# Kernel tuning notes

Hardware: AMD Instinct MI355X
Metric: run time of the kernel (lower is better)

Reference implementation:

```python
import jax, jax.numpy as jnp
import numpy as np
import math

N_HEADS = 16


def _rope(t, cos, sin):
    # t: [B, S, H, d_k] with d_k paired as (even, odd) -> complex multiply by cos+i*sin
    B, S, H, dk = t.shape
    t = t.reshape(B, S, H, dk // 2, 2)
    t0, t1 = t[..., 0], t[..., 1]
    c = cos[None, :S, None, :]
    s = sin[None, :S, None, :]
    out = jnp.stack([t0 * c - t1 * s, t0 * s + t1 * c], axis=-1)
    return out.reshape(B, S, H, dk)


def setup_inputs() -> dict:
    key = jax.random.key(0)
    ks = jax.random.split(key, 6)
    B, S, D = 2, 2048, 2048
    dk = D // N_HEADS  # 128
    x = jax.random.normal(ks[0], (B, S, D), dtype=jnp.float32)
    # standard RoPE angle table
    inv_freq = 1.0 / (10000.0 ** (np.arange(0, dk, 2, dtype=np.float32) / dk))  # [dk/2]
    t = np.arange(S, dtype=np.float32)
    ang = np.outer(t, inv_freq)  # [S, dk/2]
    freqs_cos = jnp.asarray(np.cos(ang), dtype=jnp.float32)
    freqs_sin = jnp.asarray(np.sin(ang), dtype=jnp.float32)
    # additive causal mask [1,1,S,S]
    causal = jnp.tril(jnp.ones((S, S), dtype=bool))
    mask = jnp.where(causal, 0.0, -1e9).astype(jnp.float32)[None, None]
    wscale = 1.0 / math.sqrt(D)
    Wq = jax.random.normal(ks[1], (D, D), dtype=jnp.float32) * wscale
    Wk = jax.random.normal(ks[2], (D, D), dtype=jnp.float32) * wscale
    Wv = jax.random.normal(ks[3], (D, D), dtype=jnp.float32) * wscale
    Wo = jax.random.normal(ks[4], (D, D), dtype=jnp.float32) * wscale
    return {"x": x, "freqs_cos": freqs_cos, "freqs_sin": freqs_sin, "mask": mask,
            "Wq": Wq, "Wk": Wk, "Wv": Wv, "Wo": Wo}


def reference(x, freqs_cos, freqs_sin, mask, Wq, Wk, Wv, Wo):
    B, S, D = x.shape
    H = N_HEADS
    dk = D // H
    scale = math.sqrt(dk)
    # nn.Linear(w) applies x @ w.T
    Q = (x @ Wq.T).reshape(B, S, H, dk)
    K = (x @ Wk.T).reshape(B, S, H, dk)
    V = (x @ Wv.T).reshape(B, S, H, dk)
    Q = _rope(Q, freqs_cos, freqs_sin)
    K = _rope(K, freqs_cos, freqs_sin)
    new_kv_cache = (K, V)  # kv_cache=None path: cache is just current K, V
    # [B, H, S, dk]
    Qh = Q.transpose(0, 2, 1, 3)
    Kh = K.transpose(0, 2, 1, 3)
    Vh = V.transpose(0, 2, 1, 3)
    scores = jnp.einsum('bhqd,bhkd->bhqk', Qh, Kh) / scale + mask
    attn = jax.nn.softmax(scores, axis=-1)  # dropout=0 (eval)
    ctx = jnp.einsum('bhqk,bhkd->bhqd', attn, Vh)
    ctx = ctx.transpose(0, 2, 1, 3).reshape(B, S, D)
    output = ctx @ Wo.T
    return output, new_kv_cache[0], new_kv_cache[1]
```

## Files before the change

### kernel.cpp

```cpp
#include <hip/hip_runtime.h>
#include <hip/hip_bf16.h>

#define SEQ   2048
#define DIM   2048
#define NH    16
#define DKH   128
#define BATCH 2
#define MROWS (BATCH * SEQ)
#define NQT   (SEQ / 64)

using bf16 = __hip_bfloat16;
typedef __attribute__((ext_vector_type(8))) short short8;
typedef __attribute__((ext_vector_type(4))) short short4v;
typedef __attribute__((ext_vector_type(4))) float floatx4;

union BfBits { bf16 h; short s; };

__device__ __forceinline__ void gl_lds16(const bf16* g, bf16* l) {
  __builtin_amdgcn_global_load_lds(
      (__attribute__((address_space(1))) void*)(g),
      (__attribute__((address_space(3))) void*)(l), 16, 0, 0);
}

#define S_BAR  __builtin_amdgcn_s_barrier()
#define VMCNT6 do { asm volatile("s_waitcnt vmcnt(6)" ::: "memory"); __builtin_amdgcn_sched_barrier(0); } while (0)
#define VMCNT0 do { asm volatile("s_waitcnt vmcnt(0)" ::: "memory"); __builtin_amdgcn_sched_barrier(0); } while (0)
#define LGKM0  do { asm volatile("s_waitcnt lgkmcnt(0)" ::: "memory"); __builtin_amdgcn_sched_barrier(0); } while (0)

__global__ __launch_bounds__(256) void cast5_kernel(const float* __restrict__ x,
                                                    const float* __restrict__ wq,
                                                    const float* __restrict__ wk,
                                                    const float* __restrict__ wv,
                                                    const float* __restrict__ wo,
                                                    bf16* __restrict__ dst,
                                                    int nX4, int nW4, int nTot) {
  int i = blockIdx.x * 256 + threadIdx.x;
  if (i >= nTot) return;
  const float* src;
  int off;
  int j = i - nX4;
  if (j < 0) { src = x; off = i; }
  else {
    int wsel = j >> 20;
    off = j & (nW4 - 1);
    src = (wsel == 0) ? wq : (wsel == 1) ? wk : (wsel == 2) ? wv : wo;
  }
  float4 v = reinterpret_cast<const float4*>(src)[off];
  __hip_bfloat162 h01, h23;
  h01.x = __float2bfloat16(v.x); h01.y = __float2bfloat16(v.y);
  h23.x = __float2bfloat16(v.z); h23.y = __float2bfloat16(v.w);
  reinterpret_cast<__hip_bfloat162*>(dst)[i * 2 + 0] = h01;
  reinterpret_cast<__hip_bfloat162*>(dst)[i * 2 + 1] = h23;
}

#define BUFE (256 * 64 + 128 * 64)

template <int ROWS>
__device__ __forceinline__ void stage_swz(const bf16* __restrict__ G, bf16* lds,
                                          int row0, int k0, int w, int l) {
  const int rr = w * 8 + (l >> 3);
  const int cc = ((l & 7) * 8) ^ ((l >> 3) * 8);
#pragma unroll
  for (int u = 0; u < ROWS / 64; ++u)
    gl_lds16(G + (size_t)(row0 + u * 64 + rr) * DIM + k0 + cc,
             lds + (u * 64 + w * 8) * 64);
}

template <int MODE>
__global__ __launch_bounds__(512, 2) void gemm256(const bf16* __restrict__ A,
                                                  const bf16* __restrict__ Bw,
                                                  bf16* __restrict__ Qraw,
                                                  float* __restrict__ Kout,
                                                  float* __restrict__ Vout) {
  __shared__ bf16 smem[3 * BUFE];

  const int t = threadIdx.x;
  const int w = t >> 6, l = t & 63;
  const int lr = l & 15, quad = l >> 4;
  const int wr = w >> 2;
  const int wc = w & 3;
  const int m0 = blockIdx.y * 256;
  const int n0g = blockIdx.x * 128;

  const int cb = ((quad * 8) ^ ((lr & 7) * 8));

  floatx4 acc[8][2];
#pragma unroll
  for (int mi = 0; mi < 8; ++mi)
#pragma unroll
    for (int nj = 0; nj < 2; ++nj) acc[mi][nj] = (floatx4){0.f, 0.f, 0.f, 0.f};

  const int NT = DIM / 64;

  stage_swz<256>(A, smem, m0, 0, w, l);
  stage_swz<128>(Bw, smem + 256 * 64, n0g, 0, w, l);
  stage_swz<256>(A, smem + BUFE, m0, 64, w, l);
  stage_swz<128>(Bw, smem + BUFE + 256 * 64, n0g, 64, w, l);
  VMCNT6;
  S_BAR;

  for (int kt = 0; kt < NT; ++kt) {
    const bf16* la = smem + (kt % 3) * BUFE;
    const bf16* lb = la + 256 * 64;
    bf16* stg = smem + ((kt + 2) % 3) * BUFE;
    const bool do_stage = (kt + 2 < NT);

    short8 bfr[2][2];
#pragma unroll
    for (int nj = 0; nj < 2; ++nj) {
      int rb = (wc * 32 + nj * 16 + lr) * 64;
      bfr[nj][0] = *reinterpret_cast<const short8*>(lb + rb + cb);
      bfr[nj][1] = *reinterpret_cast<const short8*>(lb + rb + (cb ^ 32));
    }
    short8 af[4][2];
#pragma unroll
    for (int i = 0; i < 4; ++i) {
      int ra = (wr * 128 + i * 16 + lr) * 64;
      af[i][0] = *reinterpret_cast<const short8*>(la + ra + cb);
      af[i][1] = *reinterpret_cast<const short8*>(la + ra + (cb ^ 32));
    }
    if (do_stage) stage_swz<256>(A, stg, m0, (kt + 2) * 64, w, l);
    LGKM0;
    __builtin_amdgcn_s_setprio(1);
#pragma unroll
    for (int i = 0; i < 4; ++i)
#pragma unroll
      for (int nj = 0; nj < 2; ++nj) {
        acc[i][nj] = __builtin_amdgcn_mfma_f32_16x16x32_bf16(
            af[i][0], bfr[nj][0], acc[i][nj], 0, 0, 0);
        acc[i][nj] = __builtin_amdgcn_mfma_f32_16x16x32_bf16(
            af[i][1], bfr[nj][1], acc[i][nj], 0, 0, 0);
      }
    __builtin_amdgcn_s_setprio(0);

#pragma unroll
    for (int i = 0; i < 4; ++i) {
      int ra = (wr * 128 + (i + 4) * 16 + lr) * 64;
      af[i][0] = *reinterpret_cast<const short8*>(la + ra + cb);
      af[i][1] = *reinterpret_cast<const short8*>(la + ra + (cb ^ 32));
    }
    if (do_stage) stage_swz<128>(Bw, stg + 256 * 64, n0g, (kt + 2) * 64, w, l);
    LGKM0;
    __builtin_amdgcn_s_setprio(1);
#pragma unroll
    for (int i = 0; i < 4; ++i)
#pragma unroll
      for (int nj = 0; nj < 2; ++nj) {
        acc[i + 4][nj] = __builtin_amdgcn_mfma_f32_16x16x32_bf16(
            af[i][0], bfr[nj][0], acc[i + 4][nj], 0, 0, 0);
        acc[i + 4][nj] = __builtin_amdgcn_mfma_f32_16x16x32_bf16(
            af[i][1], bfr[nj][1], acc[i + 4][nj], 0, 0, 0);
      }
    __builtin_amdgcn_s_setprio(0);

    if (do_stage) { VMCNT6; } else { VMCNT0; }
    S_BAR;
  }

#pragma unroll
  for (int mi = 0; mi < 8; ++mi)
#pragma unroll
    for (int nj = 0; nj < 2; ++nj) {
      int rg = m0 + wr * 128 + mi * 16 + quad * 4;
      if constexpr (MODE == 0) {
        const int region = n0g >> 11;
        int lcol = (n0g & 2047) + wc * 32 + nj * 16 + lr;
#pragma unroll
        for (int rr2 = 0; rr2 < 4; ++rr2) {
          size_t idx = (size_t)(rg + rr2) * DIM + lcol;
          if (region == 0)      Qraw[idx] = __float2bfloat16(acc[mi][nj][rr2]);
          else if (region == 1) Kout[idx] = acc[mi][nj][rr2];
          else                  Vout[idx] = acc[mi][nj][rr2];
        }
      } else {
        int lcol = n0g + wc * 32 + nj * 16 + lr;
#pragma unroll
        for (int rr2 = 0; rr2 < 4; ++rr2)
          Kout[(size_t)(rg + rr2) * DIM + lcol] = acc[mi][nj][rr2];
      }
    }
}

__global__ __launch_bounds__(256) void rope_q(const bf16* __restrict__ Qraw,
                                              const float* __restrict__ cosT,
                                              const float* __restrict__ sinT,
                                              bf16* __restrict__ Qb) {
  int g = blockIdx.x * 256 + threadIdx.x;
  int p = g & 63;
  int r = g >> 6;
  int h = r & 15;
  int s = (r >> 4) & (SEQ - 1);
  int b = r >> 15;
  __hip_bfloat162 v = reinterpret_cast<const __hip_bfloat162*>(Qraw)[g];
  float x0 = __bfloat162float(v.x), x1 = __bfloat162float(v.y);
  float c = cosT[s * 64 + p], sn = sinT[s * 64 + p];
  __hip_bfloat162 o;
  o.x = __float2bfloat16(x0 * c - x1 * sn);
  o.y = __float2bfloat16(x0 * sn + x1 * c);
  reinterpret_cast<__hip_bfloat162*>(Qb)[((size_t)(b * NH + h) * SEQ + s) * 64 + p] = o;
}

__global__ __launch_bounds__(256) void rope_k(float* __restrict__ Kf,
                                              const float* __restrict__ cosT,
                                              const float* __restrict__ sinT,
                                              bf16* __restrict__ Kb) {
  int g = blockIdx.x * 256 + threadIdx.x;
  int p = g & 63;
  int r = g >> 6;
  int h = r & 15;
  int s = (r >> 4) & (SEQ - 1);
  int b = r >> 15;
  float2 v = reinterpret_cast<const float2*>(Kf)[g];
  float c = cosT[s * 64 + p], sn = sinT[s * 64 + p];
  float o0 = v.x * c - v.y * sn;
  float o1 = v.x * sn + v.y * c;
  reinterpret_cast<float2*>(Kf)[g] = make_float2(o0, o1);
  __hip_bfloat162 ob;
  ob.x = __float2bfloat16(o0);
  ob.y = __float2bfloat16(o1);
  reinterpret_cast<__hip_bfloat162*>(Kb)[((size_t)(b * NH + h) * SEQ + s) * 64 + p] = ob;
}

__global__ __launch_bounds__(256) void vt_kernel(const float* __restrict__ V,
                                                 bf16* __restrict__ Vt) {
  __shared__ float tile[32][33];
  const int s0 = blockIdx.x * 32;
  const int d0 = blockIdx.y * 32;
  const int bh = blockIdx.z;
  const int b = bh >> 4, h = bh & 15;
  const int t = threadIdx.x;
  const int row = t >> 3, c4 = (t & 7) * 4;

  float4 v = *reinterpret_cast<const float4*>(
      V + (size_t)(b * SEQ + s0 + row) * DIM + h * DKH + d0 + c4);
  tile[row][c4 + 0] = v.x; tile[row][c4 + 1] = v.y;
  tile[row][c4 + 2] = v.z; tile[row][c4 + 3] = v.w;
  __syncthreads();

  short4v ov;
#pragma unroll
  for (int i = 0; i < 4; ++i) {
    BfBits u; u.h = __float2bfloat16(tile[c4 + i][row]);
    ov[i] = u.s;
  }
  *reinterpret_cast<short4v*>(Vt + ((size_t)(b * NH + h) * DKH + d0 + row) * SEQ + s0 + c4) = ov;
}

__global__ __launch_bounds__(256) void attn_mfma(const bf16* __restrict__ Qb,
                                                 const bf16* __restrict__ Kb,
                                                 const bf16* __restrict__ Vt,
                                                 bf16* __restrict__ ctx) {
  const int bx = blockIdx.x;
  const int h = blockIdx.y;
  const int b = blockIdx.z;
  const int t = threadIdx.x;
  const int w = t >> 6, lane = t & 63;
  const int lr = lane & 15, quad = lane >> 4;

  __shared__ short Ks[64 * 136];
  __shared__ short Vs[128 * 72];
  __shared__ short Ps[4 * 16 * 72];

  const float scale2 = 0.08838834764831845f * 1.44269504f;
  const float THR = 11.5413f;
  const size_t headQK = (size_t)(b * NH + h) * SEQ * DKH;

  for (int pass = 0; pass < 2; ++pass) {
    const int qt = pass ? bx : (NQT - 1 - bx);

    short8 qa[4];
    {
      const short* qbase = (const short*)Qb + headQK + (size_t)(qt * 64 + w * 16 + lr) * DKH;
#pragma unroll
      for (int kk = 0; kk < 4; ++kk)
        qa[kk] = *reinterpret_cast<const short8*>(qbase + kk * 32 + quad * 8);
    }

    floatx4 o[8];
#pragma unroll
    for (int n = 0; n < 8; ++n) o[n] = (floatx4){0.f, 0.f, 0.f, 0.f};
    float m[4] = {-1e30f, -1e30f, -1e30f, -1e30f};
    float l[4] = {0.f, 0.f, 0.f, 0.f};

    for (int kt = 0; kt <= qt; ++kt) {
      {
        const short* kbase = (const short*)Kb + headQK + (size_t)(kt * 64) * DKH;
#pragma unroll
        for (int u = 0; u < 4; ++u) {
          int c = t + 256 * u;
          *reinterpret_cast<int4*>(Ks + (c >> 4) * 136 + (c & 15) * 8) =
              *reinterpret_cast<const int4*>(kbase + c * 8);
        }
        const short* vbase = (const short*)Vt + (size_t)(b * NH + h) * DKH * SEQ + kt * 64;
#pragma unroll
        for (int u = 0; u < 4; ++u) {
          int c = t + 256 * u;
          *reinterpret_cast<int4*>(Vs + (c >> 3) * 72 + (c & 7) * 8) =
              *reinterpret_cast<const int4*>(vbase + (size_t)(c >> 3) * SEQ + (c & 7) * 8);
        }
      }
      __syncthreads();

      floatx4 sj[4];
#pragma unroll
      for (int j = 0; j < 4; ++j) sj[j] = (floatx4){0.f, 0.f, 0.f, 0.f};
#pragma unroll
      for (int j = 0; j < 4; ++j)
#pragma unroll
        for (int kk = 0; kk < 4; ++kk) {
          short8 kb = *reinterpret_cast<const short8*>(Ks + (j * 16 + lr) * 136 + kk * 32 + quad * 8);
          sj[j] = __builtin_amdgcn_mfma_f32_16x16x32_bf16(qa[kk], kb, sj[j], 0, 0, 0);
        }

      float sc[4][4];
#pragma unroll
      for (int j = 0; j < 4; ++j)
#pragma unroll
        for (int r = 0; r < 4; ++r) sc[j][r] = sj[j][r] * scale2;
      if (kt == qt) {
#pragma unroll
        for (int j = 0; j < 4; ++j) {
          int col = kt * 64 + j * 16 + lr;
#pragma unroll
          for (int r = 0; r < 4; ++r) {
            int rowg = qt * 64 + w * 16 + quad * 4 + r;
            if (col > rowg) sc[j][r] = -1e9f;
          }
        }
      }

#pragma unroll
      for (int r = 0; r < 4; ++r) {
        float mx = fmaxf(fmaxf(sc[0][r], sc[1][r]), fmaxf(sc[2][r], sc[3][r]));
        mx = fmaxf(mx, __shfl_xor(mx, 1, 16));
        mx = fmaxf(mx, __shfl_xor(mx, 2, 16));
        mx = fmaxf(mx, __shfl_xor(mx, 4, 16));
        mx = fmaxf(mx, __shfl_xor(mx, 8, 16));
        if (!__all(mx - m[r] <= THR)) {
          float mnew = fmaxf(m[r], mx);
          float alpha = __builtin_amdgcn_exp2f(m[r] - mnew);
          l[r] *= alpha;
#pragma unroll
          for (int n = 0; n < 8; ++n) o[n][r] *= alpha;
          m[r] = mnew;
        }
        float rs = 0.f;
#pragma unroll
        for (int j = 0; j < 4; ++j) {
          float p = __builtin_amdgcn_exp2f(sc[j][r] - m[r]);
          rs += p;
          BfBits u; u.h = __float2bfloat16(p);
          Ps[(w * 16 + quad * 4 + r) * 72 + j * 16 + lr] = u.s;
        }
        rs += __shfl_xor(rs, 1, 16);
        rs += __shfl_xor(rs, 2, 16);
        rs += __shfl_xor(rs, 4, 16);
        rs += __shfl_xor(rs, 8, 16);
        l[r] += rs;
      }

      short8 pa0 = *reinterpret_cast<const short8*>(Ps + (w * 16 + lr) * 72 + quad * 8);
      short8 pa1 = *reinterpret_cast<const short8*>(Ps + (w * 16 + lr) * 72 + 32 + quad * 8);
#pragma unroll
      for (int n = 0; n < 8; ++n) {
        short8 vb0 = *reinterpret_cast<const short8*>(Vs + (n * 16 + lr) * 72 + quad * 8);
        short8 vb1 = *reinterpret_cast<const short8*>(Vs + (n * 16 + lr) * 72 + 32 + quad * 8);
        o[n] = __builtin_amdgcn_mfma_f32_16x16x32_bf16(pa0, vb0, o[n], 0, 0, 0);
        o[n] = __builtin_amdgcn_mfma_f32_16x16x32_bf16(pa1, vb1, o[n], 0, 0, 0);
      }
      __syncthreads();
    }

    float inv[4];
#pragma unroll
    for (int r = 0; r < 4; ++r) inv[r] = 1.0f / l[r];
#pragma unroll
    for (int r = 0; r < 4; ++r) {
      size_t mrow = (size_t)b * SEQ + qt * 64 + w * 16 + quad * 4 + r;
      bf16* dst = ctx + mrow * DIM + h * DKH;
#pragma unroll
      for (int n = 0; n < 8; ++n)
        dst[n * 16 + lr] = __float2bfloat16(o[n][r] * inv[r]);
    }
  }
}

extern "C" void kernel_launch(void* const* d_in, const int* in_sizes, int n_in,
                              void* d_out, int out_size, void* d_ws, size_t ws_size,
                              hipStream_t stream) {
  const float* x = (const float*)d_in[0];
  const float* fcos = (const float*)d_in[1];
  const float* fsin = (const float*)d_in[2];
  const float* Wq = (const float*)d_in[4];
  const float* Wk = (const float*)d_in[5];
  const float* Wv = (const float*)d_in[6];
  const float* Wo = (const float*)d_in[7];

  float* out = (float*)d_out;
  float* Kout = out + (size_t)MROWS * DIM;
  float* Vout = Kout + (size_t)MROWS * DIM;

  const size_t MD = (size_t)MROWS * DIM;
  const size_t DD = (size_t)DIM * DIM;
  bf16* xb   = (bf16*)d_ws;
  bf16* Wqb  = xb + MD;
  bf16* Wkb  = Wqb + DD;
  bf16* Wvb  = Wkb + DD;
  bf16* Wob  = Wvb + DD;
  bf16* Qraw = Wob + DD;
  bf16* Qb   = Qraw + MD;
  bf16* Kb   = Qb + MD;
  bf16* Vt   = Kb + MD;
  bf16* ctxb = Qraw;

  const int nXD4 = MROWS * DIM / 4;
  const int nWD4 = DIM * DIM / 4;
  const int nTot = nXD4 + 4 * nWD4;
  cast5_kernel<<<nTot / 256, 256, 0, stream>>>(x, Wq, Wk, Wv, Wo, xb, nXD4, nWD4, nTot);

  dim3 gq(3 * DIM / 128, MROWS / 256);
  gemm256<0><<<gq, 512, 0, stream>>>(xb, Wqb, Qraw, Kout, Vout);

  const int npairs = MROWS * DIM / 2;
  rope_q<<<npairs / 256, 256, 0, stream>>>(Qraw, fcos, fsin, Qb);
  rope_k<<<npairs / 256, 256, 0, stream>>>(Kout, fcos, fsin, Kb);

  dim3 gv(SEQ / 32, DKH / 32, BATCH * NH);
  vt_kernel<<<gv, 256, 0, stream>>>(Vout, Vt);

  dim3 ga(NQT / 2, NH, BATCH);
  attn_mfma<<<ga, 256, 0, stream>>>(Qb, Kb, Vt, ctxb);

  dim3 go(DIM / 128, MROWS / 256);
  gemm256<1><<<go, 512, 0, stream>>>(ctxb, Wob, (bf16*)nullptr, out, (float*)nullptr);
}
```

Baseline: 468.7 us.

## Double-buffer K/V tiles in attention with XOR swizzle and merge post-processing kernels

The attention kernel now prefetches the next K/V tile into registers and stores it into a second LDS buffer while the current tile is consumed, so global load latency overlaps MFMA work. Padded LDS rows are replaced with an XOR swizzle to avoid bank conflicts without padding. The RoPE-Q, RoPE-K and V-transpose kernels are merged into one launch with block-index dispatch to cut launch overhead. The cost is more registers and doubled K/V LDS use, which may lower occupancy.

```diff
diff --git a/kernel.cpp b/kernel.cpp
--- a/kernel.cpp
+++ b/kernel.cpp
@@ -181,69 +181,76 @@
     }
 }
 
-__global__ __launch_bounds__(256) void rope_q(const bf16* __restrict__ Qraw,
-                                              const float* __restrict__ cosT,
-                                              const float* __restrict__ sinT,
-                                              bf16* __restrict__ Qb) {
-  int g = blockIdx.x * 256 + threadIdx.x;
-  int p = g & 63;
-  int r = g >> 6;
-  int h = r & 15;
-  int s = (r >> 4) & (SEQ - 1);
-  int b = r >> 15;
-  __hip_bfloat162 v = reinterpret_cast<const __hip_bfloat162*>(Qraw)[g];
-  float x0 = __bfloat162float(v.x), x1 = __bfloat162float(v.y);
-  float c = cosT[s * 64 + p], sn = sinT[s * 64 + p];
-  __hip_bfloat162 o;
-  o.x = __float2bfloat16(x0 * c - x1 * sn);
-  o.y = __float2bfloat16(x0 * sn + x1 * c);
-  reinterpret_cast<__hip_bfloat162*>(Qb)[((size_t)(b * NH + h) * SEQ + s) * 64 + p] = o;
-}
-
-__global__ __launch_bounds__(256) void rope_k(float* __restrict__ Kf,
-                                              const float* __restrict__ cosT,
-                                              const float* __restrict__ sinT,
-                                              bf16* __restrict__ Kb) {
-  int g = blockIdx.x * 256 + threadIdx.x;
-  int p = g & 63;
-  int r = g >> 6;
-  int h = r & 15;
-  int s = (r >> 4) & (SEQ - 1);
-  int b = r >> 15;
-  float2 v = reinterpret_cast<const float2*>(Kf)[g];
-  float c = cosT[s * 64 + p], sn = sinT[s * 64 + p];
-  float o0 = v.x * c - v.y * sn;
-  float o1 = v.x * sn + v.y * c;
-  reinterpret_cast<float2*>(Kf)[g] = make_float2(o0, o1);
-  __hip_bfloat162 ob;
-  ob.x = __float2bfloat16(o0);
-  ob.y = __float2bfloat16(o1);
-  reinterpret_cast<__hip_bfloat162*>(Kb)[((size_t)(b * NH + h) * SEQ + s) * 64 + p] = ob;
-}
-
-__global__ __launch_bounds__(256) void vt_kernel(const float* __restrict__ V,
-                                                 bf16* __restrict__ Vt) {
-  __shared__ float tile[32][33];
-  const int s0 = blockIdx.x * 32;
-  const int d0 = blockIdx.y * 32;
-  const int bh = blockIdx.z;
-  const int b = bh >> 4, h = bh & 15;
-  const int t = threadIdx.x;
-  const int row = t >> 3, c4 = (t & 7) * 4;
-
-  float4 v = *reinterpret_cast<const float4*>(
-      V + (size_t)(b * SEQ + s0 + row) * DIM + h * DKH + d0 + c4);
-  tile[row][c4 + 0] = v.x; tile[row][c4 + 1] = v.y;
-  tile[row][c4 + 2] = v.z; tile[row][c4 + 3] = v.w;
-  __syncthreads();
-
-  short4v ov;
-#pragma unroll
-  for (int i = 0; i < 4; ++i) {
-    BfBits u; u.h = __float2bfloat16(tile[c4 + i][row]);
-    ov[i] = u.s;
-  }
-  *reinterpret_cast<short4v*>(Vt + ((size_t)(b * NH + h) * DKH + d0 + row) * SEQ + s0 + c4) = ov;
+#define NRB ((MROWS * DIM / 2) / 256)
+
+__global__ __launch_bounds__(256) void postproc(const bf16* __restrict__ Qraw,
+                                                float* __restrict__ Kf,
+                                                const float* __restrict__ cosT,
+                                                const float* __restrict__ sinT,
+                                                bf16* __restrict__ Qb,
+                                                bf16* __restrict__ Kb,
+                                                const float* __restrict__ V,
+                                                bf16* __restrict__ Vt) {
+  int bid = blockIdx.x;
+  if (bid < NRB) {
+    int g = bid * 256 + threadIdx.x;
+    int p = g & 63;
+    int r = g >> 6;
+    int h = r & 15;
+    int s = (r >> 4) & (SEQ - 1);
+    int b = r >> 15;
+    __hip_bfloat162 v = reinterpret_cast<const __hip_bfloat162*>(Qraw)[g];
+    float x0 = __bfloat162float(v.x), x1 = __bfloat162float(v.y);
+    float c = cosT[s * 64 + p], sn = sinT[s * 64 + p];
+    __hip_bfloat162 o;
+    o.x = __float2bfloat16(x0 * c - x1 * sn);
+    o.y = __float2bfloat16(x0 * sn + x1 * c);
+    reinterpret_cast<__hip_bfloat162*>(Qb)[((size_t)(b * NH + h) * SEQ + s) * 64 + p] = o;
+    return;
+  }
+  bid -= NRB;
+  if (bid < NRB) {
+    int g = bid * 256 + threadIdx.x;
+    int p = g & 63;
+    int r = g >> 6;
+    int h = r & 15;
+    int s = (r >> 4) & (SEQ - 1);
+    int b = r >> 15;
+    float2 v = reinterpret_cast<const float2*>(Kf)[g];
+    float c = cosT[s * 64 + p], sn = sinT[s * 64 + p];
+    float o0 = v.x * c - v.y * sn;
+    float o1 = v.x * sn + v.y * c;
+    reinterpret_cast<float2*>(Kf)[g] = make_float2(o0, o1);
+    __hip_bfloat162 ob;
+    ob.x = __float2bfloat16(o0);
+    ob.y = __float2bfloat16(o1);
+    reinterpret_cast<__hip_bfloat162*>(Kb)[((size_t)(b * NH + h) * SEQ + s) * 64 + p] = ob;
+    return;
+  }
+  bid -= NRB;
+  {
+    __shared__ float tile[32][33];
+    const int s0 = (bid & 63) * 32;
+    const int d0 = ((bid >> 6) & 3) * 32;
+    const int bh = bid >> 8;
+    const int b = bh >> 4, h = bh & 15;
+    const int t = threadIdx.x;
+    const int row = t >> 3, c4 = (t & 7) * 4;
+
+    float4 v = *reinterpret_cast<const float4*>(
+        V + (size_t)(b * SEQ + s0 + row) * DIM + h * DKH + d0 + c4);
+    tile[row][c4 + 0] = v.x; tile[row][c4 + 1] = v.y;
+    tile[row][c4 + 2] = v.z; tile[row][c4 + 3] = v.w;
+    __syncthreads();
+
+    short4v ov;
+#pragma unroll
+    for (int i = 0; i < 4; ++i) {
+      BfBits u; u.h = __float2bfloat16(tile[c4 + i][row]);
+      ov[i] = u.s;
+    }
+    *reinterpret_cast<short4v*>(Vt + ((size_t)(b * NH + h) * DKH + d0 + row) * SEQ + s0 + c4) = ov;
+  }
 }
 
 __global__ __launch_bounds__(256) void attn_mfma(const bf16* __restrict__ Qb,
@@ -256,14 +263,38 @@
   const int t = threadIdx.x;
   const int w = t >> 6, lane = t & 63;
   const int lr = lane & 15, quad = lane >> 4;
-
-  __shared__ short Ks[64 * 136];
-  __shared__ short Vs[128 * 72];
+  const int kswz = 8 * (lr & 7);
+
+  __shared__ short Ks[2][64 * 128];
+  __shared__ short Vs[2][128 * 64];
   __shared__ short Ps[4 * 16 * 72];
 
   const float scale2 = 0.08838834764831845f * 1.44269504f;
   const float THR = 11.5413f;
   const size_t headQK = (size_t)(b * NH + h) * SEQ * DKH;
+  const short* kbase0 = (const short*)Kb + headQK;
+  const short* vbase0 = (const short*)Vt + (size_t)(b * NH + h) * DKH * SEQ;
+
+  int4 kreg[4], vreg[4];
+
+  auto LD = [&](int kt) {
+#pragma unroll
+    for (int u = 0; u < 4; ++u) {
+      int c = t + 256 * u;
+      kreg[u] = *reinterpret_cast<const int4*>(kbase0 + (size_t)(kt * 64) * DKH + c * 8);
+      vreg[u] = *reinterpret_cast<const int4*>(vbase0 + kt * 64 + (size_t)(c >> 3) * SEQ + (c & 7) * 8);
+    }
+  };
+  auto ST = [&](int buf) {
+#pragma unroll
+    for (int u = 0; u < 4; ++u) {
+      int c = t + 256 * u;
+      int krow = c >> 4, kcol = ((c & 15) * 8) ^ (8 * (krow & 7));
+      *reinterpret_cast<int4*>(&Ks[buf][krow * 128 + kcol]) = kreg[u];
+      int vrow = c >> 3, vcol = ((c & 7) * 8) ^ (8 * (vrow & 7));
+      *reinterpret_cast<int4*>(&Vs[buf][vrow * 64 + vcol]) = vreg[u];
+    }
+  };
 
   for (int pass = 0; pass < 2; ++pass) {
     const int qt = pass ? bx : (NQT - 1 - bx);
@@ -282,24 +313,19 @@
     float m[4] = {-1e30f, -1e30f, -1e30f, -1e30f};
     float l[4] = {0.f, 0.f, 0.f, 0.f};
 
+    LD(0);
+    ST(0);
+    if (qt >= 1) LD(1);
+    __syncthreads();
+
     for (int kt = 0; kt <= qt; ++kt) {
-      {
-        const short* kbase = (const short*)Kb + headQK + (size_t)(kt * 64) * DKH;
-#pragma unroll
-        for (int u = 0; u < 4; ++u) {
-          int c = t + 256 * u;
-          *reinterpret_cast<int4*>(Ks + (c >> 4) * 136 + (c & 15) * 8) =
-              *reinterpret_cast<const int4*>(kbase + c * 8);
-        }
-        const short* vbase = (const short*)Vt + (size_t)(b * NH + h) * DKH * SEQ + kt * 64;
-#pragma unroll
-        for (int u = 0; u < 4; ++u) {
-          int c = t + 256 * u;
-          *reinterpret_cast<int4*>(Vs + (c >> 3) * 72 + (c & 7) * 8) =
-              *reinterpret_cast<const int4*>(vbase + (size_t)(c >> 3) * SEQ + (c & 7) * 8);
-        }
-      }
-      __syncthreads();
+      const int cur = kt & 1;
+      if (kt + 1 <= qt) {
+        ST(cur ^ 1);
+        if (kt + 2 <= qt) LD(kt + 2);
+      }
+      const short* ksb = Ks[cur];
+      const short* vsb = Vs[cur];
 
       floatx4 sj[4];
 #pragma unroll
@@ -308,7 +334,8 @@
       for (int j = 0; j < 4; ++j)
 #pragma unroll
         for (int kk = 0; kk < 4; ++kk) {
-          short8 kb = *reinterpret_cast<const short8*>(Ks + (j * 16 + lr) * 136 + kk * 32 + quad * 8);
+          short8 kb = *reinterpret_cast<const short8*>(
+              ksb + (j * 16 + lr) * 128 + ((kk * 32 + quad * 8) ^ kswz));
           sj[j] = __builtin_amdgcn_mfma_f32_16x16x32_bf16(qa[kk], kb, sj[j], 0, 0, 0);
         }
 
@@ -363,8 +390,10 @@
       short8 pa1 = *reinterpret_cast<const short8*>(Ps + (w * 16 + lr) * 72 + 32 + quad * 8);
 #pragma unroll
       for (int n = 0; n < 8; ++n) {
-        short8 vb0 = *reinterpret_cast<const short8*>(Vs + (n * 16 + lr) * 72 + quad * 8);
-        short8 vb1 = *reinterpret_cast<const short8*>(Vs + (n * 16 + lr) * 72 + 32 + quad * 8);
+        short8 vb0 = *reinterpret_cast<const short8*>(
+            vsb + (n * 16 + lr) * 64 + ((quad * 8) ^ kswz));
+        short8 vb1 = *reinterpret_cast<const short8*>(
+            vsb + (n * 16 + lr) * 64 + ((32 + quad * 8) ^ kswz));
         o[n] = __builtin_amdgcn_mfma_f32_16x16x32_bf16(pa0, vb0, o[n], 0, 0, 0);
         o[n] = __builtin_amdgcn_mfma_f32_16x16x32_bf16(pa1, vb1, o[n], 0, 0, 0);
       }
@@ -421,12 +450,7 @@
   dim3 gq(3 * DIM / 128, MROWS / 256);
   gemm256<0><<<gq, 512, 0, stream>>>(xb, Wqb, Qraw, Kout, Vout);
 
-  const int npairs = MROWS * DIM / 2;
-  rope_q<<<npairs / 256, 256, 0, stream>>>(Qraw, fcos, fsin, Qb);
-  rope_k<<<npairs / 256, 256, 0, stream>>>(Kout, fcos, fsin, Kb);
-
-  dim3 gv(SEQ / 32, DKH / 32, BATCH * NH);
-  vt_kernel<<<gv, 256, 0, stream>>>(Vout, Vt);
+  postproc<<<2 * NRB + 8192, 256, 0, stream>>>(Qraw, Kout, fcos, fsin, Qb, Kb, Vout, Vt);
 
   dim3 ga(NQT / 2, NH, BATCH);
   attn_mfma<<<ga, 256, 0, stream>>>(Qb, Kb, Vt, ctxb);
```

Result: slower. 524.1 us (+11.8%).
